# Kernel tuning notes

Measured on AMD Instinct MI355X. Metric: run time of the kernel, lower is better.

## Reference

```python
import jax, jax.numpy as jnp
import numpy as np

B, T, D, H = 512, 1024, 64, 128

def setup_inputs() -> dict:
    key = jax.random.key(0)
    ks = jax.random.split(key, 9)
    s_ih = 1.0 / np.sqrt(H)
    inp = {
        "x_seq": jax.random.normal(ks[0], (B, T, D), dtype=jnp.float32),
        # PyTorch LSTM params, gate order (i, f, g, o)
        "W_ih": jax.random.uniform(ks[1], (4 * H, D), minval=-s_ih, maxval=s_ih, dtype=jnp.float32),
        "W_hh": jax.random.uniform(ks[2], (4 * H, H), minval=-s_ih, maxval=s_ih, dtype=jnp.float32),
        "b_ih": jax.random.uniform(ks[3], (4 * H,), minval=-s_ih, maxval=s_ih, dtype=jnp.float32),
        "b_hh": jax.random.uniform(ks[4], (4 * H,), minval=-s_ih, maxval=s_ih, dtype=jnp.float32),
        # fc head: Linear(H,64) -> ReLU -> Linear(64,1)
        "W1": jax.random.uniform(ks[5], (64, H), minval=-s_ih, maxval=s_ih, dtype=jnp.float32),
        "b1": jax.random.uniform(ks[6], (64,), minval=-s_ih, maxval=s_ih, dtype=jnp.float32),
        "W2": jax.random.uniform(ks[7], (1, 64), minval=-0.125, maxval=0.125, dtype=jnp.float32),
        "b2": jax.random.uniform(ks[8], (1,), minval=-0.125, maxval=0.125, dtype=jnp.float32),
    }
    return inp


def _lstm_last(x_seq, W_ih, W_hh, b_ih, b_hh):
    # Precompute input projections for all timesteps in one big GEMM: [T,B,4H]
    xg = jnp.einsum('btd,gd->tbg', x_seq, W_ih) + b_ih + b_hh
    h0 = jnp.zeros((x_seq.shape[0], W_hh.shape[1]), dtype=x_seq.dtype)
    c0 = jnp.zeros_like(h0)
    Hd = W_hh.shape[1]

    def step(carry, xg_t):
        h, c = carry
        gates = xg_t + h @ W_hh.T  # [B,4H], gate order i,f,g,o
        i = jax.nn.sigmoid(gates[:, 0 * Hd:1 * Hd])
        f = jax.nn.sigmoid(gates[:, 1 * Hd:2 * Hd])
        g = jnp.tanh(gates[:, 2 * Hd:3 * Hd])
        o = jax.nn.sigmoid(gates[:, 3 * Hd:4 * Hd])
        c_new = f * c + i * g
        h_new = o * jnp.tanh(c_new)
        return (h_new, c_new), None

    (h_last, _), _ = jax.lax.scan(step, (h0, c0), xg)
    return h_last  # [B,H] == out[:, -1, :]


def reference(x_seq, W_ih, W_hh, b_ih, b_hh, W1, b1, W2, b2):
    h_last = _lstm_last(x_seq, W_ih, W_hh, b_ih, b_hh)
    z = jax.nn.relu(h_last @ W1.T + b1)
    y = z @ W2.T + b2  # [B,1]
    return y[:, 0]
```

## Files before the change

### kernel.cpp

```cpp
#include <hip/hip_runtime.h>


#define BB 512
#define TT 1024
#define DD 64
#define HH 128
#define KK 192

typedef _Float16 half2_t __attribute__((ext_vector_type(2)));

__device__ __forceinline__ float dot2(half2_t a, half2_t b, float c) {
    asm("v_dot2_f32_f16 %0, %1, %2, %0" : "+v"(c) : "v"(a), "v"(b));
    return c;
}

__device__ __forceinline__ half2_t pack2(float a, float b) {
    half2_t r;
    r[0] = (_Float16)a;
    r[1] = (_Float16)b;
    return r;
}

__device__ __forceinline__ half2_t bc(unsigned int u) {
    return __builtin_bit_cast(half2_t, u);
}

__device__ __forceinline__ float sigm(float x) {
    return 1.f / (1.f + __expf(-x));
}
__device__ __forceinline__ float tanh_f(float x) {
    return 1.f - 2.f / (__expf(2.f * x) + 1.f);
}

__device__ __forceinline__ half2_t wld(const float* __restrict__ Whh,
                                       const float* __restrict__ Wih,
                                       int gate, int k) {
    if (k < HH) return pack2(Whh[gate * HH + k], Whh[gate * HH + k + 1]);
    return pack2(Wih[gate * DD + (k - HH)], Wih[gate * DD + (k - HH) + 1]);
}

__global__ __launch_bounds__(1024, 4)
void lstm_fused_kernel(const float* __restrict__ x_seq,
                       const float* __restrict__ W_ih,
                       const float* __restrict__ W_hh,
                       const float* __restrict__ b_ih,
                       const float* __restrict__ b_hh,
                       const float* __restrict__ W1v,
                       const float* __restrict__ b1v,
                       const float* __restrict__ W2v,
                       const float* __restrict__ b2v,
                       float* __restrict__ out)
{
    const int tid = threadIdx.x;
    const int q   = tid & 3;
    const int g   = tid >> 2;
    const int b0  = blockIdx.x * 2;

    __shared__ __align__(16) _Float16 hx[2][2][KK];
    __shared__ __align__(16) float    gl[2][4 * HH];

    const int k0 = q * 48;
    half2_t wa[24], wb[24];
#pragma unroll
    for (int j = 0; j < 24; ++j) {
        wa[j] = wld(W_hh, W_ih, g,       k0 + 2 * j);
        wb[j] = wld(W_hh, W_ih, g + 256, k0 + 2 * j);
    }
    const float biasA = b_ih[g] + b_hh[g];
    const float biasB = b_ih[g + 256] + b_hh[g + 256];

    if (tid < 256) hx[0][tid >> 7][tid & 127] = (_Float16)0.f;
    if (tid < 128) {
        const int r = tid >> 6, k = tid & 63;
        hx[0][r][HH + k] = (_Float16)x_seq[((b0 + r) * TT + 0) * DD + k];
    }
    float c_reg = 0.f;
    const int pr = (tid - 896) >> 6;
    const int pk = (tid - 896) & 63;
    __syncthreads();

    for (int t = 0; t < TT; ++t) {
        const int cur = t & 1;

        float xpre = 0.f;
        const bool do_pre = (t + 1 < TT) && (tid >= 896);
        if (do_pre) xpre = x_seq[((b0 + pr) * TT + (t + 1)) * DD + pk];

        const uint4* s0 = reinterpret_cast<const uint4*>(&hx[cur][0][k0]);
        const uint4* s1 = reinterpret_cast<const uint4*>(&hx[cur][1][k0]);
        float aA0 = 0.f, aA1 = 0.f, aB0 = 0.f, aB1 = 0.f;
#pragma unroll
        for (int j = 0; j < 6; ++j) {
            const uint4 v0 = s0[j];
            const uint4 v1 = s1[j];
            aA0 = dot2(wa[4 * j + 0], bc(v0.x), aA0);
            aA1 = dot2(wa[4 * j + 0], bc(v1.x), aA1);
            aB0 = dot2(wb[4 * j + 0], bc(v0.x), aB0);
            aB1 = dot2(wb[4 * j + 0], bc(v1.x), aB1);
            aA0 = dot2(wa[4 * j + 1], bc(v0.y), aA0);
            aA1 = dot2(wa[4 * j + 1], bc(v1.y), aA1);
            aB0 = dot2(wb[4 * j + 1], bc(v0.y), aB0);
            aB1 = dot2(wb[4 * j + 1], bc(v1.y), aB1);
            aA0 = dot2(wa[4 * j + 2], bc(v0.z), aA0);
            aA1 = dot2(wa[4 * j + 2], bc(v1.z), aA1);
            aB0 = dot2(wb[4 * j + 2], bc(v0.z), aB0);
            aB1 = dot2(wb[4 * j + 2], bc(v1.z), aB1);
            aA0 = dot2(wa[4 * j + 3], bc(v0.w), aA0);
            aA1 = dot2(wa[4 * j + 3], bc(v1.w), aA1);
            aB0 = dot2(wb[4 * j + 3], bc(v0.w), aB0);
            aB1 = dot2(wb[4 * j + 3], bc(v1.w), aB1);
        }

        aA0 += __shfl_xor(aA0, 1, 64); aA0 += __shfl_xor(aA0, 2, 64);
        aA1 += __shfl_xor(aA1, 1, 64); aA1 += __shfl_xor(aA1, 2, 64);
        aB0 += __shfl_xor(aB0, 1, 64); aB0 += __shfl_xor(aB0, 2, 64);
        aB1 += __shfl_xor(aB1, 1, 64); aB1 += __shfl_xor(aB1, 2, 64);

        const float v  = (q == 0) ? aA0 : (q == 1) ? aA1 : (q == 2) ? aB0 : aB1;
        const float bb = (q < 2) ? biasA : biasB;
        const int   row = q & 1;
        const int   gg  = (q < 2) ? g : g + 256;
        gl[row][gg] = v + bb;
        __syncthreads();

        if (tid < 256) {
            const int r = tid >> 7, u = tid & 127;
            const float gi = gl[r][u];
            const float gf = gl[r][HH + u];
            const float gG = gl[r][2 * HH + u];
            const float go = gl[r][3 * HH + u];
            c_reg = sigm(gf) * c_reg + sigm(gi) * tanh_f(gG);
            hx[cur ^ 1][r][u] = (_Float16)(sigm(go) * tanh_f(c_reg));
        }
        if (do_pre) hx[cur ^ 1][pr][HH + pk] = (_Float16)xpre;
        __syncthreads();
    }

    if (tid < 128) {
        const int r = tid >> 6, j = tid & 63;
        float z = b1v[j];
        const float* w1 = W1v + j * HH;
#pragma unroll 16
        for (int k = 0; k < HH; ++k)
            z = fmaf(w1[k], (float)hx[0][r][k], z);
        z = fmaxf(z, 0.f) * W2v[j];
#pragma unroll
        for (int off = 32; off; off >>= 1)
            z += __shfl_down(z, off, 64);
        if (j == 0) out[b0 + r] = z + b2v[0];
    }
}

extern "C" void kernel_launch(void* const* d_in, const int* in_sizes, int n_in,
                              void* d_out, int out_size, void* d_ws, size_t ws_size,
                              hipStream_t stream) {
    const float* x_seq = (const float*)d_in[0];
    const float* W_ih  = (const float*)d_in[1];
    const float* W_hh  = (const float*)d_in[2];
    const float* b_ih  = (const float*)d_in[3];
    const float* b_hh  = (const float*)d_in[4];
    const float* W1    = (const float*)d_in[5];
    const float* b1    = (const float*)d_in[6];
    const float* W2    = (const float*)d_in[7];
    const float* b2    = (const float*)d_in[8];
    float* out = (float*)d_out;

    lstm_fused_kernel<<<BB / 2, 1024, 0, stream>>>(
        x_seq, W_ih, W_hh, b_ih, b_hh, W1, b1, W2, b2, out);
}
```

Measured before the change: 1.487 ms.

## Remap LSTM gate work so each quad owns all four gates, dropping one barrier

Threads are regrouped so that a quad of lanes holds the i, f, g and o rows for one hidden unit, split over two K halves. Partial sums are combined with DPP lane swaps, and the cell update is computed redundantly in registers. This removes the shared gate buffer and one __syncthreads per timestep, and the block shrinks from 1024 to 512 threads. In exchange each thread holds twice as many weight registers (96 half2) and does more dot products per step, which raises register pressure and per-thread latency on the serial recurrence.

Measured after the change: 1.899 ms. +27.7%, slower.

```diff
diff --git a/kernel.cpp b/kernel.cpp
--- a/kernel.cpp
+++ b/kernel.cpp
@@ -1,7 +1,6 @@
 #include <hip/hip_runtime.h>
 
 
-#define BB 512
 #define TT 1024
 #define DD 64
 #define HH 128
@@ -14,15 +13,19 @@
     return c;
 }
 
-__device__ __forceinline__ half2_t pack2(float a, float b) {
-    half2_t r;
-    r[0] = (_Float16)a;
-    r[1] = (_Float16)b;
-    return r;
+__device__ __forceinline__ half2_t bc(unsigned int u) {
+    return __builtin_bit_cast(half2_t, u);
 }
 
-__device__ __forceinline__ half2_t bc(unsigned int u) {
-    return __builtin_bit_cast(half2_t, u);
+__device__ __forceinline__ float dpp_add_xor1(float x) {
+    int y = __builtin_amdgcn_update_dpp(0, __builtin_bit_cast(int, x),
+                                        0xB1, 0xF, 0xF, true);
+    return x + __builtin_bit_cast(float, y);
+}
+__device__ __forceinline__ float dpp_mov_xor2(float x) {
+    int y = __builtin_amdgcn_update_dpp(0, __builtin_bit_cast(int, x),
+                                        0x4E, 0xF, 0xF, true);
+    return __builtin_bit_cast(float, y);
 }
 
 __device__ __forceinline__ float sigm(float x) {
@@ -35,11 +38,16 @@
 __device__ __forceinline__ half2_t wld(const float* __restrict__ Whh,
                                        const float* __restrict__ Wih,
                                        int gate, int k) {
-    if (k < HH) return pack2(Whh[gate * HH + k], Whh[gate * HH + k + 1]);
-    return pack2(Wih[gate * DD + (k - HH)], Wih[gate * DD + (k - HH) + 1]);
+    float2 f;
+    if (k < HH) f = *reinterpret_cast<const float2*>(Whh + gate * HH + k);
+    else        f = *reinterpret_cast<const float2*>(Wih + gate * DD + (k - HH));
+    half2_t r;
+    r[0] = (_Float16)f.x;
+    r[1] = (_Float16)f.y;
+    return r;
 }
 
-__global__ __launch_bounds__(1024, 4)
+__global__ __launch_bounds__(512, 2)
 void lstm_fused_kernel(const float* __restrict__ x_seq,
                        const float* __restrict__ W_ih,
                        const float* __restrict__ W_hh,
@@ -52,87 +60,96 @@
                        float* __restrict__ out)
 {
     const int tid = threadIdx.x;
-    const int q   = tid & 3;
-    const int g   = tid >> 2;
+    const int q   = tid & 1;
+    const int e   = (tid >> 1) & 1;
+    const int u   = tid >> 2;
     const int b0  = blockIdx.x * 2;
 
     __shared__ __align__(16) _Float16 hx[2][2][KK];
-    __shared__ __align__(16) float    gl[2][4 * HH];
 
-    const int k0 = q * 48;
-    half2_t wa[24], wb[24];
+    const int g0 = u + e * 256;
+    const int g1 = u + 128 + e * 256;
+    const int kb = q * 96;
+    half2_t w0[48], w1[48];
 #pragma unroll
-    for (int j = 0; j < 24; ++j) {
-        wa[j] = wld(W_hh, W_ih, g,       k0 + 2 * j);
-        wb[j] = wld(W_hh, W_ih, g + 256, k0 + 2 * j);
+    for (int j = 0; j < 48; ++j) {
+        w0[j] = wld(W_hh, W_ih, g0, kb + 2 * j);
+        w1[j] = wld(W_hh, W_ih, g1, kb + 2 * j);
     }
-    const float biasA = b_ih[g] + b_hh[g];
-    const float biasB = b_ih[g + 256] + b_hh[g + 256];
+    const float bI = b_ih[u]       + b_hh[u];
+    const float bF = b_ih[u + 128] + b_hh[u + 128];
+    const float bG = b_ih[u + 256] + b_hh[u + 256];
+    const float bO = b_ih[u + 384] + b_hh[u + 384];
 
     if (tid < 256) hx[0][tid >> 7][tid & 127] = (_Float16)0.f;
     if (tid < 128) {
         const int r = tid >> 6, k = tid & 63;
         hx[0][r][HH + k] = (_Float16)x_seq[((b0 + r) * TT + 0) * DD + k];
     }
-    float c_reg = 0.f;
-    const int pr = (tid - 896) >> 6;
-    const int pk = (tid - 896) & 63;
+    float c0 = 0.f, c1 = 0.f;
+
+    const bool is_pre = (q == 1) && (e == 1);
+    const int  xr = u & 1, xk = u >> 1;
     __syncthreads();
 
     for (int t = 0; t < TT; ++t) {
-        const int cur = t & 1;
+        const int cur = t & 1, nxt = cur ^ 1;
 
         float xpre = 0.f;
-        const bool do_pre = (t + 1 < TT) && (tid >= 896);
-        if (do_pre) xpre = x_seq[((b0 + pr) * TT + (t + 1)) * DD + pk];
+        const bool pre = is_pre && (t + 1 < TT);
+        if (pre) xpre = x_seq[((b0 + xr) * TT + (t + 1)) * DD + xk];
 
-        const uint4* s0 = reinterpret_cast<const uint4*>(&hx[cur][0][k0]);
-        const uint4* s1 = reinterpret_cast<const uint4*>(&hx[cur][1][k0]);
-        float aA0 = 0.f, aA1 = 0.f, aB0 = 0.f, aB1 = 0.f;
+        const uint4* s0 = reinterpret_cast<const uint4*>(&hx[cur][0][0]) + q * 12;
+        const uint4* s1 = reinterpret_cast<const uint4*>(&hx[cur][1][0]) + q * 12;
+
+        float a00 = 0.f, a01 = 0.f, a10 = 0.f, a11 = 0.f;
 #pragma unroll
-        for (int j = 0; j < 6; ++j) {
+        for (int j = 0; j < 12; ++j) {
             const uint4 v0 = s0[j];
             const uint4 v1 = s1[j];
-            aA0 = dot2(wa[4 * j + 0], bc(v0.x), aA0);
-            aA1 = dot2(wa[4 * j + 0], bc(v1.x), aA1);
-            aB0 = dot2(wb[4 * j + 0], bc(v0.x), aB0);
-            aB1 = dot2(wb[4 * j + 0], bc(v1.x), aB1);
-            aA0 = dot2(wa[4 * j + 1], bc(v0.y), aA0);
-            aA1 = dot2(wa[4 * j + 1], bc(v1.y), aA1);
-            aB0 = dot2(wb[4 * j + 1], bc(v0.y), aB0);
-            aB1 = dot2(wb[4 * j + 1], bc(v1.y), aB1);
-            aA0 = dot2(wa[4 * j + 2], bc(v0.z), aA0);
-            aA1 = dot2(wa[4 * j + 2], bc(v1.z), aA1);
-            aB0 = dot2(wb[4 * j + 2], bc(v0.z), aB0);
-            aB1 = dot2(wb[4 * j + 2], bc(v1.z), aB1);
-            aA0 = dot2(wa[4 * j + 3], bc(v0.w), aA0);
-            aA1 = dot2(wa[4 * j + 3], bc(v1.w), aA1);
-            aB0 = dot2(wb[4 * j + 3], bc(v0.w), aB0);
-            aB1 = dot2(wb[4 * j + 3], bc(v1.w), aB1);
+            a00 = dot2(w0[4 * j + 0], bc(v0.x), a00);
+            a01 = dot2(w0[4 * j + 0], bc(v1.x), a01);
+            a10 = dot2(w1[4 * j + 0], bc(v0.x), a10);
+            a11 = dot2(w1[4 * j + 0], bc(v1.x), a11);
+            a00 = dot2(w0[4 * j + 1], bc(v0.y), a00);
+            a01 = dot2(w0[4 * j + 1], bc(v1.y), a01);
+            a10 = dot2(w1[4 * j + 1], bc(v0.y), a10);
+            a11 = dot2(w1[4 * j + 1], bc(v1.y), a11);
+            a00 = dot2(w0[4 * j + 2], bc(v0.z), a00);
+            a01 = dot2(w0[4 * j + 2], bc(v1.z), a01);
+            a10 = dot2(w1[4 * j + 2], bc(v0.z), a10);
+            a11 = dot2(w1[4 * j + 2], bc(v1.z), a11);
+            a00 = dot2(w0[4 * j + 3], bc(v0.w), a00);
+            a01 = dot2(w0[4 * j + 3], bc(v1.w), a01);
+            a10 = dot2(w1[4 * j + 3], bc(v0.w), a10);
+            a11 = dot2(w1[4 * j + 3], bc(v1.w), a11);
         }
 
-        aA0 += __shfl_xor(aA0, 1, 64); aA0 += __shfl_xor(aA0, 2, 64);
-        aA1 += __shfl_xor(aA1, 1, 64); aA1 += __shfl_xor(aA1, 2, 64);
-        aB0 += __shfl_xor(aB0, 1, 64); aB0 += __shfl_xor(aB0, 2, 64);
-        aB1 += __shfl_xor(aB1, 1, 64); aB1 += __shfl_xor(aB1, 2, 64);
+        a00 = dpp_add_xor1(a00);
+        a01 = dpp_add_xor1(a01);
+        a10 = dpp_add_xor1(a10);
+        a11 = dpp_add_xor1(a11);
+        const float o00 = dpp_mov_xor2(a00);
+        const float o01 = dpp_mov_xor2(a01);
+        const float o10 = dpp_mov_xor2(a10);
+        const float o11 = dpp_mov_xor2(a11);
 
-        const float v  = (q == 0) ? aA0 : (q == 1) ? aA1 : (q == 2) ? aB0 : aB1;
-        const float bb = (q < 2) ? biasA : biasB;
-        const int   row = q & 1;
-        const int   gg  = (q < 2) ? g : g + 256;
-        gl[row][gg] = v + bb;
-        __syncthreads();
+        const float gi0 = (e ? o00 : a00) + bI;
+        const float gi1 = (e ? o01 : a01) + bI;
+        const float gf0 = (e ? o10 : a10) + bF;
+        const float gf1 = (e ? o11 : a11) + bF;
+        const float gg0 = (e ? a00 : o00) + bG;
+        const float gg1 = (e ? a01 : o01) + bG;
+        const float go0 = (e ? a10 : o10) + bO;
+        const float go1 = (e ? a11 : o11) + bO;
 
-        if (tid < 256) {
-            const int r = tid >> 7, u = tid & 127;
-            const float gi = gl[r][u];
-            const float gf = gl[r][HH + u];
-            const float gG = gl[r][2 * HH + u];
-            const float go = gl[r][3 * HH + u];
-            c_reg = sigm(gf) * c_reg + sigm(gi) * tanh_f(gG);
-            hx[cur ^ 1][r][u] = (_Float16)(sigm(go) * tanh_f(c_reg));
-        }
-        if (do_pre) hx[cur ^ 1][pr][HH + pk] = (_Float16)xpre;
+        c0 = sigm(gf0) * c0 + sigm(gi0) * tanh_f(gg0);
+        c1 = sigm(gf1) * c1 + sigm(gi1) * tanh_f(gg1);
+        const float h0n = sigm(go0) * tanh_f(c0);
+        const float h1n = sigm(go1) * tanh_f(c1);
+
+        if (e == 0) hx[nxt][q][u] = (_Float16)(q ? h1n : h0n);
+        if (pre)    hx[nxt][xr][HH + xk] = (_Float16)xpre;
         __syncthreads();
     }
 
@@ -165,6 +182,6 @@
     const float* b2    = (const float*)d_in[8];
     float* out = (float*)d_out;
 
-    lstm_fused_kernel<<<BB / 2, 1024, 0, stream>>>(
+    lstm_fused_kernel<<<256, 512, 0, stream>>>(
         x_seq, W_ih, W_hh, b_ih, b_hh, W1, b1, W2, b2, out);
 }
```
